# Optimization experiments

Measured on AMD Instinct MI355X. Metric: run time of the kernel, lower is better.

## Reference

```python
import jax, jax.numpy as jnp
import numpy as np

N, F, H, K, E = 10000, 128, 128, 500, 320000
EPS = 1e-15


def setup_inputs() -> dict:
    key = jax.random.key(0)
    ks = jax.random.split(key, 16)
    def lin(k, fi, fo):
        return jax.random.normal(k, (fi, fo), jnp.float32) / np.sqrt(fi).astype(np.float32)
    inp = {
        'nodes': jax.random.normal(ks[0], (N, F), jnp.float32),
        'edges': jax.random.randint(ks[1], (2, E), 0, N, jnp.int32),
        'batch': jnp.zeros((N,), jnp.int32),
        'W1': lin(ks[2], F, H), 'b1': jnp.zeros((H,), jnp.float32),
        'W2': lin(ks[3], H, H), 'b2': jnp.zeros((H,), jnp.float32),
        'pool_W': lin(ks[4], H, K), 'pool_b': jnp.zeros((K,), jnp.float32),
        'W3': lin(ks[5], H, H), 'b3': jnp.zeros((H,), jnp.float32),
        'W4': lin(ks[6], H, H), 'b4': jnp.zeros((H,), jnp.float32),
        'W5': lin(ks[7], H, F), 'b5': jnp.zeros((F,), jnp.float32),
    }
    return inp


def reference(nodes, edges, batch, W1, b1, W2, b2, pool_W, pool_b, W3, b3, W4, b4, W5, b5):
    n = nodes.shape[0]
    row, col = edges[0], edges[1]
    # GCN normalization with self-loops (computed once, shared by all convs)
    loop = jnp.arange(n, dtype=row.dtype)
    row_sl = jnp.concatenate([row, loop])
    col_sl = jnp.concatenate([col, loop])
    deg = jax.ops.segment_sum(jnp.ones_like(col_sl, dtype=nodes.dtype), col_sl, num_segments=n)
    dinv = jnp.where(deg > 0, 1.0 / jnp.sqrt(deg), 0.0)
    norm = dinv[row_sl] * dinv[col_sl]  # [E+N]

    def gcn(x, W, b):
        h = x @ W
        msg = h[row_sl] * norm[:, None]
        return jax.ops.segment_sum(msg, col_sl, num_segments=n) + b

    x = jnp.tanh(gcn(nodes, W1, b1))
    x = jnp.tanh(gcn(x, W2, b2))

    # dense batch (single graph) + dense adjacency [1, N, N]
    adj = jnp.zeros((n, n), x.dtype).at[row, col].add(1.0)[None]
    xd = x[None]                                   # [1, N, H]
    s_logits = xd @ pool_W + pool_b                # [1, N, K]

    # ---- dense_mincut_pool ----
    s = jax.nn.softmax(s_logits, axis=-1)
    k = s.shape[-1]
    out = jnp.einsum('bnk,bnh->bkh', s, xd)        # s^T x, [1, K, H]
    a_s = adj @ s                                  # [1, N, K]
    out_adj = jnp.swapaxes(s, 1, 2) @ a_s          # s^T A s, [1, K, K]
    mincut_num = jnp.trace(out_adj, axis1=1, axis2=2)
    d_flat = adj.sum(-1)                           # [1, N]
    # trace(s^T D s) = sum_n d_n * sum_k s_nk^2
    mincut_den = jnp.einsum('bn,bnk,bnk->b', d_flat, s, s) + EPS
    mincut_loss = jnp.mean(-(mincut_num / mincut_den))
    ss = jnp.swapaxes(s, 1, 2) @ s                 # [1, K, K]
    ss_norm = jnp.linalg.norm(ss, axis=(-1, -2), keepdims=True)
    i_s_normed = jnp.eye(k, dtype=ss.dtype) / jnp.sqrt(jnp.asarray(k, ss.dtype))
    ortho_loss = jnp.mean(jnp.linalg.norm(ss / (ss_norm + EPS) - i_s_normed, axis=(-1, -2)))
    # zero diagonal, then symmetric degree normalization
    out_adj = out_adj * (1.0 - jnp.eye(k, dtype=out_adj.dtype))
    d = jnp.sqrt(out_adj.sum(-1))[:, None] + EPS   # [1, 1, K]
    out_adj = out_adj / d / jnp.swapaxes(d, 1, 2)
    # ---- end pool ----

    s2 = jax.nn.softmax(s_logits, axis=-1)
    x_out = (s2 @ out)[0]                          # [N, H]
    adj_out = s2 @ (out_adj @ jnp.swapaxes(s2, 1, 2))  # [1, N, N]

    # recon_adj = False -> reuse original edge_index
    x = jnp.tanh(gcn(x_out, W3, b3))
    x = jnp.tanh(gcn(x, W4, b4))
    x = gcn(x, W5, b5)
    return x, adj_out, mincut_loss, ortho_loss
```

## Files before the change

kernel.cpp:

```cpp
#include <hip/hip_runtime.h>
#include <hip/hip_bf16.h>
#include <math.h>

#define EPSF 1e-15f

typedef __attribute__((ext_vector_type(8))) short bf16x8;
typedef __attribute__((ext_vector_type(4))) float f32x4;

__device__ __forceinline__ void gload_lds16(const void* g, void* l){
  __builtin_amdgcn_global_load_lds(
    (const __attribute__((address_space(1))) unsigned int*)(g),
    (__attribute__((address_space(3))) unsigned int*)(l), 16, 0, 0);
}


__global__ void k_count_deg(const int* __restrict__ edges, int E, int* indeg, int* outdeg){
  int e = blockIdx.x*blockDim.x + threadIdx.x;
  if (e >= E) return;
  int r = edges[e], c = edges[E+e];
  atomicAdd(&outdeg[r], 1);
  atomicAdd(&indeg[c], 1);
}

__global__ void k_dinv(const int* __restrict__ indeg, float* __restrict__ dinv, int N){
  int i = blockIdx.x*blockDim.x + threadIdx.x;
  if (i >= N) return;
  dinv[i] = rsqrtf((float)(indeg[i] + 1));
}

__global__ void k_scan_block(const int* __restrict__ cnt, int* __restrict__ rowptr, int n){
  __shared__ int csum[257];
  const int T = 256;
  int chunk = (n + T - 1)/T;
  int t = threadIdx.x;
  int beg = t*chunk, end = min(n, beg + chunk);
  int s = 0;
  for (int i = beg; i < end; ++i) s += cnt[i];
  csum[t+1] = s;
  if (t == 0) csum[0] = 0;
  __syncthreads();
  if (t == 0){ for (int i = 1; i <= T; ++i) csum[i] += csum[i-1]; }
  __syncthreads();
  int acc = csum[t];
  for (int i = beg; i < end; ++i){ rowptr[i] = acc; acc += cnt[i]; }
  if (t == T-1) rowptr[n] = csum[T];
}

__global__ void k_fill_csr(const int* __restrict__ edges, int E, int* cur_in, int* cur_out,
                           int* __restrict__ src, int* __restrict__ dst){
  int e = blockIdx.x*blockDim.x + threadIdx.x;
  if (e >= E) return;
  int r = edges[e], c = edges[E+e];
  int p = atomicAdd(&cur_in[c], 1);  src[p] = r;
  int q = atomicAdd(&cur_out[r], 1); dst[q] = c;
}

__global__ __launch_bounds__(128)
void k_gcn_agg_b(const __hip_bfloat16* __restrict__ hb, const float* __restrict__ dinv,
                 const int* __restrict__ rowptr, const int* __restrict__ src,
                 const float* __restrict__ bias, float* __restrict__ outf,
                 __hip_bfloat16* __restrict__ outb, int Hd, int do_tanh){
  int c = blockIdx.x;
  int t = threadIdx.x;
  float dc = dinv[c];
  float sum = __bfloat162float(hb[(size_t)c*Hd + t]) * dc;
  int e0 = rowptr[c], e1 = rowptr[c+1];
  for (int e = e0; e < e1; ++e){
    int sidx = src[e];
    sum += __bfloat162float(hb[(size_t)sidx*Hd + t]) * dinv[sidx];
  }
  float v = sum * dc + bias[t];
  if (do_tanh) v = tanhf(v);
  if (outf) outf[(size_t)c*Hd + t] = v;
  if (outb) outb[(size_t)c*Hd + t] = __float2bfloat16(v);
}

__global__ __launch_bounds__(256)
void k_as_agg_b2(const __hip_bfloat16* __restrict__ sb, const int* __restrict__ rowptr,
                 const int* __restrict__ dst, float* __restrict__ a_s, int K2, int KP2){
  int n = blockIdx.x;
  int e0 = rowptr[n], e1 = rowptr[n+1];
  const unsigned* sb32 = (const unsigned*)sb;
  for (int k = threadIdx.x; k < K2; k += blockDim.x){
    float a0 = 0.f, a1 = 0.f;
    for (int e = e0; e < e1; ++e){
      unsigned v = sb32[(size_t)dst[e]*KP2 + k];
      a0 += __uint_as_float(v << 16);
      a1 += __uint_as_float(v & 0xFFFF0000u);
    }
    float2* o = (float2*)(a_s + (size_t)n*(K2*2));
    o[k] = make_float2(a0, a1);
  }
}

__global__ void k_pack_bf16pad(const float* __restrict__ x, __hip_bfloat16* __restrict__ y,
                               int rows, int K, int KP){
  long long n = (long long)rows*KP;
  for (long long i = (long long)blockIdx.x*blockDim.x + threadIdx.x; i < n;
       i += (long long)gridDim.x*blockDim.x){
    int row = (int)(i / KP), col = (int)(i - (long long)row*KP);
    y[i] = (col < K) ? __float2bfloat16(x[(size_t)row*K + col]) : __float2bfloat16(0.f);
  }
}

__global__ __launch_bounds__(256)
void k_transpose_f2b(const float* __restrict__ X, __hip_bfloat16* __restrict__ XT,
                     int R, int C, int Cp, int Np){
  __shared__ float t[32][33];
  int jb = blockIdx.x*32;
  int ib = blockIdx.y*32;
  int tx = threadIdx.x & 31, ty = threadIdx.x >> 5;
  #pragma unroll
  for (int k = 0; k < 4; ++k){
    int i = ib + ty + k*8, j = jb + tx;
    t[ty + k*8][tx] = (i < R && j < C) ? X[(size_t)i*C + j] : 0.f;
  }
  __syncthreads();
  #pragma unroll
  for (int k = 0; k < 4; ++k){
    int jr = jb + ty + k*8, ic = ib + tx;
    if (jr < Cp && ic < Np)
      XT[(size_t)jr*Np + ic] = __float2bfloat16(t[tx][ty + k*8]);
  }
}

#define MT 128
#define NT 128
#define KT 32
__global__ __launch_bounds__(256)
void k_gemm_abt_mfma(const short* __restrict__ A, const short* __restrict__ B,
                     const float* __restrict__ bias,
                     float* __restrict__ Cf, __hip_bfloat16* __restrict__ Cb,
                     int M, int Nd, int KP, int ldcb, int swz){
  __shared__ __align__(16) short Asl[128*32];
  __shared__ __align__(16) short Bsl[128*32];
  int bx = blockIdx.x, by = blockIdx.y;
  if (swz){
    int gx = gridDim.x;
    int nwg = gx * gridDim.y;
    int bid = by*gx + bx;
    int q = nwg >> 3, r = nwg & 7;
    int xcd = bid & 7, o = bid >> 3;
    int nb = (xcd < r ? xcd*(q+1) : r*(q+1) + (xcd - r)*q) + o;
    bx = nb % gx; by = nb / gx;
  }
  int tid = threadIdx.x;
  int lane = tid & 63, wave = tid >> 6;
  int wr = wave >> 1, wc = wave & 1;
  int l15 = lane & 15, l4 = lane >> 4;
  int tM = by * MT, tN = bx * NT;

  f32x4 acc[4][4];
  #pragma unroll
  for (int i = 0; i < 4; ++i)
    #pragma unroll
    for (int j = 0; j < 4; ++j) acc[i][j] = (f32x4){0.f,0.f,0.f,0.f};

  const short* gA0 = A + (size_t)(tM + (tid>>2))*KP + (tid&3)*8;
  const short* gA1 = A + (size_t)(tM + 64 + (tid>>2))*KP + (tid&3)*8;
  const short* gB0 = B + (size_t)(tN + (tid>>2))*KP + (tid&3)*8;
  const short* gB1 = B + (size_t)(tN + 64 + (tid>>2))*KP + (tid&3)*8;
  short* lA0 = Asl + wave*512;
  short* lA1 = Asl + 2048 + wave*512;
  short* lB0 = Bsl + wave*512;
  short* lB1 = Bsl + 2048 + wave*512;

  for (int k0 = 0; k0 < KP; k0 += KT){
    __syncthreads();
    gload_lds16(gA0 + k0, lA0);
    gload_lds16(gA1 + k0, lA1);
    gload_lds16(gB0 + k0, lB0);
    gload_lds16(gB1 + k0, lB1);
    __syncthreads();

    bf16x8 af[4], bfr[4];
    #pragma unroll
    for (int mi = 0; mi < 4; ++mi)
      af[mi] = *(const bf16x8*)(Asl + (wr*64 + mi*16 + l15)*32 + l4*8);
    #pragma unroll
    for (int nj = 0; nj < 4; ++nj)
      bfr[nj] = *(const bf16x8*)(Bsl + (wc*64 + nj*16 + l15)*32 + l4*8);
    #pragma unroll
    for (int mi = 0; mi < 4; ++mi)
      #pragma unroll
      for (int nj = 0; nj < 4; ++nj)
        acc[mi][nj] = __builtin_amdgcn_mfma_f32_16x16x32_bf16(af[mi], bfr[nj], acc[mi][nj], 0, 0, 0);
  }

  #pragma unroll
  for (int mi = 0; mi < 4; ++mi){
    #pragma unroll
    for (int r = 0; r < 4; ++r){
      int gr = tM + wr*64 + mi*16 + l4*4 + r;
      if (gr >= M) continue;
      #pragma unroll
      for (int nj = 0; nj < 4; ++nj){
        int gc = tN + wc*64 + nj*16 + l15;
        if (gc >= Nd) continue;
        float v = acc[mi][nj][r];
        if (bias) v += bias[gc];
        if (Cf) Cf[(size_t)gr*Nd + gc] = v;
        else    Cb[(size_t)gr*ldcb + gc] = __float2bfloat16(v);
      }
    }
  }
}

__global__ __launch_bounds__(256)
void k_gemm_abt_mfma_sk(const short* __restrict__ A, const short* __restrict__ B,
                        float* __restrict__ C, int M, int Nd, int ldC,
                        int KL, int kChunk){
  __shared__ __align__(16) short Asl[128*32];
  __shared__ __align__(16) short Bsl[128*32];
  int tid = threadIdx.x;
  int lane = tid & 63, wave = tid >> 6;
  int wr = wave >> 1, wc = wave & 1;
  int l15 = lane & 15, l4 = lane >> 4;
  int tM = blockIdx.y * MT, tN = blockIdx.x * NT;
  int kBeg = blockIdx.z * kChunk;
  int kEnd = min(KL, kBeg + kChunk);

  f32x4 acc[4][4];
  #pragma unroll
  for (int i = 0; i < 4; ++i)
    #pragma unroll
    for (int j = 0; j < 4; ++j) acc[i][j] = (f32x4){0.f,0.f,0.f,0.f};

  const short* gA0 = A + (size_t)(tM + (tid>>2))*KL + (tid&3)*8;
  const short* gA1 = A + (size_t)(tM + 64 + (tid>>2))*KL + (tid&3)*8;
  const short* gB0 = B + (size_t)(tN + (tid>>2))*KL + (tid&3)*8;
  const short* gB1 = B + (size_t)(tN + 64 + (tid>>2))*KL + (tid&3)*8;
  short* lA0 = Asl + wave*512;
  short* lA1 = Asl + 2048 + wave*512;
  short* lB0 = Bsl + wave*512;
  short* lB1 = Bsl + 2048 + wave*512;

  for (int k0 = kBeg; k0 < kEnd; k0 += KT){
    __syncthreads();
    gload_lds16(gA0 + k0, lA0);
    gload_lds16(gA1 + k0, lA1);
    gload_lds16(gB0 + k0, lB0);
    gload_lds16(gB1 + k0, lB1);
    __syncthreads();

    bf16x8 af[4], bfr[4];
    #pragma unroll
    for (int mi = 0; mi < 4; ++mi)
      af[mi] = *(const bf16x8*)(Asl + (wr*64 + mi*16 + l15)*32 + l4*8);
    #pragma unroll
    for (int nj = 0; nj < 4; ++nj)
      bfr[nj] = *(const bf16x8*)(Bsl + (wc*64 + nj*16 + l15)*32 + l4*8);
    #pragma unroll
    for (int mi = 0; mi < 4; ++mi)
      #pragma unroll
      for (int nj = 0; nj < 4; ++nj)
        acc[mi][nj] = __builtin_amdgcn_mfma_f32_16x16x32_bf16(af[mi], bfr[nj], acc[mi][nj], 0, 0, 0);
  }

  #pragma unroll
  for (int mi = 0; mi < 4; ++mi){
    #pragma unroll
    for (int r = 0; r < 4; ++r){
      int gr = tM + wr*64 + mi*16 + l4*4 + r;
      if (gr >= M) continue;
      #pragma unroll
      for (int nj = 0; nj < 4; ++nj){
        int gc = tN + wc*64 + nj*16 + l15;
        if (gc >= Nd) continue;
        atomicAdd(&C[(size_t)gr*ldC + gc], acc[mi][nj][r]);
      }
    }
  }
}


__global__ __launch_bounds__(256)
void k_softmax(float* __restrict__ s, __hip_bfloat16* __restrict__ sb,
               const int* __restrict__ outdeg,
               float* __restrict__ scalars, int N, int K, int KP){
  int wid = threadIdx.x >> 6, lane = threadIdx.x & 63;
  int row = blockIdx.x*4 + wid;
  if (row >= N) return;
  float* sr = s + (size_t)row*K;
  __hip_bfloat16* sbr = sb + (size_t)row*KP;
  float v[8];
  float m = -INFINITY;
  #pragma unroll
  for (int i = 0; i < 8; ++i){
    int k = lane + i*64;
    v[i] = (k < K) ? sr[k] : -INFINITY;
    m = fmaxf(m, v[i]);
  }
  for (int off = 32; off; off >>= 1) m = fmaxf(m, __shfl_xor(m, off));
  float sum = 0.f;
  #pragma unroll
  for (int i = 0; i < 8; ++i){
    int k = lane + i*64;
    if (k < K){ v[i] = expf(v[i] - m); sum += v[i]; } else v[i] = 0.f;
  }
  for (int off = 32; off; off >>= 1) sum += __shfl_xor(sum, off);
  float inv = 1.f / sum;
  float ssq = 0.f;
  #pragma unroll
  for (int i = 0; i < 8; ++i){
    int k = lane + i*64;
    if (k < K){
      float p = v[i]*inv;
      sr[k] = p;
      sbr[k] = __float2bfloat16(p);
      ssq += p*p;
    }
  }
  for (int off = 32; off; off >>= 1) ssq += __shfl_xor(ssq, off);
  if (lane == 0) atomicAdd(&scalars[1], (float)outdeg[row] * ssq);
}

__global__ void k_trace(const float* __restrict__ P, float* __restrict__ scalars, int K){
  float t = 0.f;
  for (int i = threadIdx.x; i < K; i += blockDim.x) t += P[(size_t)i*K + i];
  for (int off = 32; off; off >>= 1) t += __shfl_xor(t, off);
  __shared__ float wsum[4];
  int lane = threadIdx.x & 63, wid = threadIdx.x >> 6;
  if (lane == 0) wsum[wid] = t;
  __syncthreads();
  if (threadIdx.x == 0) scalars[0] = wsum[0]+wsum[1]+wsum[2]+wsum[3];
}

__global__ void k_reduce_sq(const float* __restrict__ x, int n, float* __restrict__ out){
  float a = 0.f;
  for (int i = blockIdx.x*blockDim.x + threadIdx.x; i < n; i += gridDim.x*blockDim.x){
    float v = x[i]; a += v*v;
  }
  for (int off = 32; off; off >>= 1) a += __shfl_xor(a, off);
  if ((threadIdx.x & 63) == 0) atomicAdd(out, a);
}

__global__ void k_ortho(const float* __restrict__ ss, const float* __restrict__ scalars,
                        int K, float* __restrict__ out){
  float inv = 1.f / (sqrtf(scalars[2]) + EPSF);
  float isk = rsqrtf((float)K);
  float a = 0.f;
  int n = K*K;
  for (int idx = blockIdx.x*blockDim.x + threadIdx.x; idx < n; idx += gridDim.x*blockDim.x){
    int i = idx / K, j = idx - i*K;
    float v = ss[idx]*inv - ((i == j) ? isk : 0.f);
    a += v*v;
  }
  for (int off = 32; off; off >>= 1) a += __shfl_xor(a, off);
  if ((threadIdx.x & 63) == 0) atomicAdd(out, a);
}

__global__ __launch_bounds__(256)
void k_rowsum_d(const float* __restrict__ P, float* __restrict__ dvec, int K){
  int wid = threadIdx.x >> 6, lane = threadIdx.x & 63;
  int row = blockIdx.x*4 + wid;
  if (row >= K) return;
  const float* pr = P + (size_t)row*K;
  float rs = 0.f;
  for (int j = lane; j < K; j += 64) if (j != row) rs += pr[j];
  for (int off = 32; off; off >>= 1) rs += __shfl_xor(rs, off);
  if (lane == 0) dvec[row] = sqrtf(rs) + EPSF;
}

__global__ void k_norm_adj(float* __restrict__ P, const float* __restrict__ dvec, int K){
  int idx = blockIdx.x*blockDim.x + threadIdx.x;
  if (idx >= K*K) return;
  int i = idx / K, j = idx - i*K;
  float v = P[idx];
  P[idx] = (i == j) ? 0.f : v / (dvec[i]*dvec[j]);
}

__global__ void k_finalize(const float* __restrict__ scalars, float* __restrict__ out2){
  if (threadIdx.x == 0){
    out2[0] = -(scalars[0] / (scalars[1] + EPSF));
    out2[1] = sqrtf(scalars[3]);
  }
}


extern "C" void kernel_launch(void* const* d_in, const int* in_sizes, int n_in,
                              void* d_out, int out_size, void* d_ws, size_t ws_size,
                              hipStream_t stream) {
  const float* nodes = (const float*)d_in[0];
  const int*   edges = (const int*)d_in[1];
  const float* W1 = (const float*)d_in[3];  const float* b1 = (const float*)d_in[4];
  const float* W2 = (const float*)d_in[5];  const float* b2 = (const float*)d_in[6];
  const float* pW = (const float*)d_in[7];  const float* pB = (const float*)d_in[8];
  const float* W3 = (const float*)d_in[9];  const float* b3 = (const float*)d_in[10];
  const float* W4 = (const float*)d_in[11]; const float* b4 = (const float*)d_in[12];
  const float* W5 = (const float*)d_in[13]; const float* b5 = (const float*)d_in[14];

  const int H = 128, F = 128, N = 10000, E = 320000, K = 500;
  const int KP = 512;
  const int NP = 10016;
  const int MP = 79*128;
  (void)n_in; (void)out_size; (void)in_sizes;

  float* out_x   = (float*)d_out;
  float* out_adj = out_x + (size_t)N*F;
  float* out_ls  = out_adj + (size_t)N*N;

  char* ws = (char*)d_ws;
  size_t off = 0;
  auto alloc = [&](size_t bytes) -> void* {
    off = (off + 255) & ~(size_t)255;
    void* p = ws + off;
    off += bytes;
    return p;
  };
  int*   deg2       = (int*)alloc((size_t)2*N*4);
  int*   indeg      = deg2;
  int*   outdeg     = deg2 + N;
  float* zf         = (float*)alloc(((size_t)K*H + 2*(size_t)K*K + 64)*4);
  float* out_pool   = zf;
  float* P          = zf + (size_t)K*H;
  float* ssm        = P + (size_t)K*K;
  float* scalars    = ssm + (size_t)K*K;
  __hip_bfloat16* sub = (__hip_bfloat16*)alloc((size_t)2*MP*KP*2);
  __hip_bfloat16* s_b = sub;
  __hip_bfloat16* u_b = sub + (size_t)MP*KP;
  int*   rowptr_in  = (int*)alloc((size_t)(N+1)*4);
  int*   rowptr_out = (int*)alloc((size_t)(N+1)*4);
  int*   cur_in     = (int*)alloc((size_t)N*4);
  int*   cur_out    = (int*)alloc((size_t)N*4);
  int*   csr_src    = (int*)alloc((size_t)E*4);
  int*   csr_dst    = (int*)alloc((size_t)E*4);
  float* dinv       = (float*)alloc((size_t)N*4);
  __hip_bfloat16* h_b  = (__hip_bfloat16*)alloc((size_t)N*H*2);
  __hip_bfloat16* nodes_b = (__hip_bfloat16*)alloc((size_t)MP*H*2);
  __hip_bfloat16* xa_b = (__hip_bfloat16*)alloc((size_t)MP*H*2);
  __hip_bfloat16* xb_b = (__hip_bfloat16*)alloc((size_t)MP*H*2);
  float* xb         = (float*)alloc((size_t)N*H*4);
  float* s          = (float*)alloc((size_t)N*K*4);
  float* a_s        = (float*)alloc((size_t)N*K*4);
  float* dvec       = (float*)alloc((size_t)K*4);
  __hip_bfloat16* Pt_b = (__hip_bfloat16*)alloc((size_t)KP*KP*2);
  __hip_bfloat16* st_b = (__hip_bfloat16*)alloc((size_t)KP*NP*2);
  __hip_bfloat16* a_st = (__hip_bfloat16*)alloc((size_t)KP*NP*2);
  __hip_bfloat16* xbt  = (__hip_bfloat16*)alloc((size_t)H*NP*2);
  __hip_bfloat16* opT  = (__hip_bfloat16*)alloc((size_t)H*KP*2);
  __hip_bfloat16* W1t  = (__hip_bfloat16*)alloc((size_t)H*F*2);
  __hip_bfloat16* W2t  = (__hip_bfloat16*)alloc((size_t)H*H*2);
  __hip_bfloat16* W3t  = (__hip_bfloat16*)alloc((size_t)H*H*2);
  __hip_bfloat16* W4t  = (__hip_bfloat16*)alloc((size_t)H*H*2);
  __hip_bfloat16* W5t  = (__hip_bfloat16*)alloc((size_t)F*H*2);
  __hip_bfloat16* pWt  = (__hip_bfloat16*)alloc((size_t)KP*H*2);
  (void)ws_size;

  hipMemsetAsync(deg2, 0, (size_t)2*N*4, stream);
  hipMemsetAsync(zf,   0, ((size_t)K*H + 2*(size_t)K*K + 64)*4, stream);
  hipMemsetAsync(sub,  0, (size_t)2*MP*KP*2, stream);

  int eb = (E + 255)/256;
  k_count_deg<<<eb, 256, 0, stream>>>(edges, E, indeg, outdeg);
  k_dinv<<<(N+255)/256, 256, 0, stream>>>(indeg, dinv, N);
  k_scan_block<<<1, 256, 0, stream>>>(indeg,  rowptr_in,  N);
  k_scan_block<<<1, 256, 0, stream>>>(outdeg, rowptr_out, N);
  hipMemcpyAsync(cur_in,  rowptr_in,  (size_t)N*4, hipMemcpyDeviceToDevice, stream);
  hipMemcpyAsync(cur_out, rowptr_out, (size_t)N*4, hipMemcpyDeviceToDevice, stream);
  k_fill_csr<<<eb, 256, 0, stream>>>(edges, E, cur_in, cur_out, csr_src, csr_dst);

  { dim3 g(4, 4);  k_transpose_f2b<<<g, 256, 0, stream>>>(W1, W1t, F, H, H, F); }
  { dim3 g(4, 4);  k_transpose_f2b<<<g, 256, 0, stream>>>(W2, W2t, H, H, H, H); }
  { dim3 g(4, 4);  k_transpose_f2b<<<g, 256, 0, stream>>>(W3, W3t, H, H, H, H); }
  { dim3 g(4, 4);  k_transpose_f2b<<<g, 256, 0, stream>>>(W4, W4t, H, H, H, H); }
  { dim3 g(4, 4);  k_transpose_f2b<<<g, 256, 0, stream>>>(W5, W5t, H, F, F, H); }
  { dim3 g(16, 4); k_transpose_f2b<<<g, 256, 0, stream>>>(pW, pWt, H, K, KP, H); }
  k_pack_bf16pad<<<1024, 256, 0, stream>>>(nodes, nodes_b, N, F, F);

  auto mfma = [&](const __hip_bfloat16* A, const __hip_bfloat16* B, const float* bias,
                  float* Cf, __hip_bfloat16* Cb, int M, int Nd, int Kp, int ldcb, int swz){
    dim3 g((Nd + NT - 1)/NT, (M + MT - 1)/MT);
    k_gemm_abt_mfma<<<g, 256, 0, stream>>>((const short*)A, (const short*)B, bias,
                                           Cf, Cb, M, Nd, Kp, ldcb, swz);
  };

  mfma(nodes_b, W1t, nullptr, nullptr, h_b, N, H, F, H, 0);
  k_gcn_agg_b<<<N, H, 0, stream>>>(h_b, dinv, rowptr_in, csr_src, b1, nullptr, xa_b, H, 1);
  mfma(xa_b, W2t, nullptr, nullptr, h_b, N, H, H, H, 0);
  k_gcn_agg_b<<<N, H, 0, stream>>>(h_b, dinv, rowptr_in, csr_src, b2, xb, xb_b, H, 1);

  mfma(xb_b, pWt, pB, s, nullptr, N, K, H, 0, 0);
  k_softmax<<<(N+3)/4, 256, 0, stream>>>(s, s_b, outdeg, scalars, N, K, KP);
  { dim3 g(KP/32, NP/32); k_transpose_f2b<<<g, 256, 0, stream>>>(s,   st_b, N, K, KP, NP); }
  k_as_agg_b2<<<N, 256, 0, stream>>>(s_b, rowptr_out, csr_dst, a_s, K/2, KP/2);
  { dim3 g(KP/32, NP/32); k_transpose_f2b<<<g, 256, 0, stream>>>(a_s, a_st, N, K, KP, NP); }
  { dim3 g(H/32,  NP/32); k_transpose_f2b<<<g, 256, 0, stream>>>(xb,  xbt,  N, H, H,  NP); }

  const int kChunk = 1280;
  { dim3 g(1, 4, 8); k_gemm_abt_mfma_sk<<<g, 256, 0, stream>>>((const short*)st_b, (const short*)xbt,
                                                               out_pool, K, H, H, NP, kChunk); }
  { dim3 g(4, 4, 8); k_gemm_abt_mfma_sk<<<g, 256, 0, stream>>>((const short*)st_b, (const short*)a_st,
                                                               P, K, K, K, NP, kChunk); }
  { dim3 g(4, 4, 8); k_gemm_abt_mfma_sk<<<g, 256, 0, stream>>>((const short*)st_b, (const short*)st_b,
                                                               ssm, K, K, K, NP, kChunk); }
  k_trace<<<1, 256, 0, stream>>>(P, scalars, K);
  k_reduce_sq<<<256, 256, 0, stream>>>(ssm, K*K, &scalars[2]);
  k_ortho<<<256, 256, 0, stream>>>(ssm, scalars, K, &scalars[3]);
  k_rowsum_d<<<(K+3)/4, 256, 0, stream>>>(P, dvec, K);
  k_norm_adj<<<(K*K+255)/256, 256, 0, stream>>>(P, dvec, K);
  k_finalize<<<1, 64, 0, stream>>>(scalars, out_ls);

  { dim3 g(KP/32, KP/32); k_transpose_f2b<<<g, 256, 0, stream>>>(P, Pt_b, K, K, KP, KP); }
  mfma(s_b, Pt_b, nullptr, nullptr, u_b, N, K, KP, KP, 0);
  mfma(u_b, s_b, nullptr, out_adj, nullptr, N, N, KP, 0, 1);
  { dim3 g(H/32, KP/32); k_transpose_f2b<<<g, 256, 0, stream>>>(out_pool, opT, K, H, H, KP); }
  mfma(s_b, opT, nullptr, nullptr, xa_b, N, H, KP, H, 0);

  mfma(xa_b, W3t, nullptr, nullptr, h_b, N, H, H, H, 0);
  k_gcn_agg_b<<<N, H, 0, stream>>>(h_b, dinv, rowptr_in, csr_src, b3, nullptr, xb_b, H, 1);
  mfma(xb_b, W4t, nullptr, nullptr, h_b, N, H, H, H, 0);
  k_gcn_agg_b<<<N, H, 0, stream>>>(h_b, dinv, rowptr_in, csr_src, b4, nullptr, xa_b, H, 1);
  mfma(xa_b, W5t, nullptr, nullptr, h_b, N, F, H, F, 0);
  k_gcn_agg_b<<<N, F, 0, stream>>>(h_b, dinv, rowptr_in, csr_src, b5, out_x, nullptr, F, 0);
}
```

Baseline: 1.021 ms.

## Batch small kernels and fuse pooling split-K GEMMs to cut launch overhead

Merges many small launches. The dinv computation and cursor copies are folded into the scan kernel. The six weight transposes become one batched launch, and two of the N-sized transposes become another. The three split-K pooling GEMMs run as a single grid, and the trace, reduce, ortho and adjacency-normalisation kernels are combined into two stats kernels. The GCN aggregation loop is also unrolled by two with dual accumulators to expose more memory parallelism. The goal is fewer launches and host API calls. The cost is branchy dispatch and some idle blocks in the batched grids.

```diff
diff --git a/kernel.cpp b/kernel.cpp
--- a/kernel.cpp
+++ b/kernel.cpp
@@ -22,13 +22,8 @@
   atomicAdd(&indeg[c], 1);
 }
 
-__global__ void k_dinv(const int* __restrict__ indeg, float* __restrict__ dinv, int N){
-  int i = blockIdx.x*blockDim.x + threadIdx.x;
-  if (i >= N) return;
-  dinv[i] = rsqrtf((float)(indeg[i] + 1));
-}
-
-__global__ void k_scan_block(const int* __restrict__ cnt, int* __restrict__ rowptr, int n){
+__global__ void k_scan_fused(const int* __restrict__ cnt, int* __restrict__ rowptr,
+                             int* __restrict__ cur, float* __restrict__ dinvOut, int n){
   __shared__ int csum[257];
   const int T = 256;
   int chunk = (n + T - 1)/T;
@@ -42,7 +37,12 @@
   if (t == 0){ for (int i = 1; i <= T; ++i) csum[i] += csum[i-1]; }
   __syncthreads();
   int acc = csum[t];
-  for (int i = beg; i < end; ++i){ rowptr[i] = acc; acc += cnt[i]; }
+  for (int i = beg; i < end; ++i){
+    rowptr[i] = acc;
+    cur[i] = acc;
+    if (dinvOut) dinvOut[i] = rsqrtf((float)(cnt[i] + 1));
+    acc += cnt[i];
+  }
   if (t == T-1) rowptr[n] = csum[T];
 }
 
@@ -64,11 +64,19 @@
   int t = threadIdx.x;
   float dc = dinv[c];
   float sum = __bfloat162float(hb[(size_t)c*Hd + t]) * dc;
+  float sum2 = 0.f;
   int e0 = rowptr[c], e1 = rowptr[c+1];
-  for (int e = e0; e < e1; ++e){
-    int sidx = src[e];
-    sum += __bfloat162float(hb[(size_t)sidx*Hd + t]) * dinv[sidx];
-  }
+  int e = e0;
+  for (; e + 1 < e1; e += 2){
+    int sa = src[e], sb2 = src[e+1];
+    sum  += __bfloat162float(hb[(size_t)sa*Hd  + t]) * dinv[sa];
+    sum2 += __bfloat162float(hb[(size_t)sb2*Hd + t]) * dinv[sb2];
+  }
+  if (e < e1){
+    int sa = src[e];
+    sum += __bfloat162float(hb[(size_t)sa*Hd + t]) * dinv[sa];
+  }
+  sum += sum2;
   float v = sum * dc + bias[t];
   if (do_tanh) v = tanhf(v);
   if (outf) outf[(size_t)c*Hd + t] = v;
@@ -103,12 +111,12 @@
   }
 }
 
-__global__ __launch_bounds__(256)
-void k_transpose_f2b(const float* __restrict__ X, __hip_bfloat16* __restrict__ XT,
-                     int R, int C, int Cp, int Np){
+__device__ __forceinline__ void transpose_tile(const float* X, __hip_bfloat16* XT,
+                                               int R, int C, int Cp, int Np,
+                                               int bx, int by){
   __shared__ float t[32][33];
-  int jb = blockIdx.x*32;
-  int ib = blockIdx.y*32;
+  int jb = bx*32;
+  int ib = by*32;
   int tx = threadIdx.x & 31, ty = threadIdx.x >> 5;
   #pragma unroll
   for (int k = 0; k < 4; ++k){
@@ -122,6 +130,38 @@
     if (jr < Cp && ic < Np)
       XT[(size_t)jr*Np + ic] = __float2bfloat16(t[tx][ty + k*8]);
   }
+}
+
+__global__ __launch_bounds__(256)
+void k_transpose_f2b(const float* __restrict__ X, __hip_bfloat16* __restrict__ XT,
+                     int R, int C, int Cp, int Np){
+  transpose_tile(X, XT, R, C, Cp, Np, blockIdx.x, blockIdx.y);
+}
+
+struct TPar { const float* src; __hip_bfloat16* dst; int R, C, Cp, Np; };
+
+__global__ __launch_bounds__(256)
+void k_transpose_batch6(TPar p0, TPar p1, TPar p2, TPar p3, TPar p4, TPar p5){
+  TPar p;
+  switch (blockIdx.z){
+    case 0: p = p0; break;
+    case 1: p = p1; break;
+    case 2: p = p2; break;
+    case 3: p = p3; break;
+    case 4: p = p4; break;
+    default: p = p5; break;
+  }
+  if ((int)blockIdx.x >= (p.Cp + 31)/32 || (int)blockIdx.y >= (p.Np + 31)/32) return;
+  transpose_tile(p.src, p.dst, p.R, p.C, p.Cp, p.Np, blockIdx.x, blockIdx.y);
+}
+
+__global__ __launch_bounds__(256)
+void k_transpose_batch2(const float* __restrict__ X0, __hip_bfloat16* __restrict__ T0,
+                        const float* __restrict__ X1, __hip_bfloat16* __restrict__ T1,
+                        int R, int C, int Cp, int Np){
+  const float* X = blockIdx.z ? X1 : X0;
+  __hip_bfloat16* XT = blockIdx.z ? T1 : T0;
+  transpose_tile(X, XT, R, C, Cp, Np, blockIdx.x, blockIdx.y);
 }
 
 #define MT 128
@@ -207,17 +247,24 @@
 }
 
 __global__ __launch_bounds__(256)
-void k_gemm_abt_mfma_sk(const short* __restrict__ A, const short* __restrict__ B,
-                        float* __restrict__ C, int M, int Nd, int ldC,
-                        int KL, int kChunk){
+void k_pool_sk(const short* __restrict__ st, const short* __restrict__ xbt,
+               const short* __restrict__ a_st,
+               float* __restrict__ out_pool, float* __restrict__ P, float* __restrict__ ssm,
+               int K, int Hd, int KL, int kChunk){
   __shared__ __align__(16) short Asl[128*32];
   __shared__ __align__(16) short Bsl[128*32];
+  int sel = blockIdx.z >> 3;
+  int chunk = blockIdx.z & 7;
+  const short* B = (sel == 0) ? xbt : (sel == 1) ? a_st : st;
+  float* C = (sel == 0) ? out_pool : (sel == 1) ? P : ssm;
+  int Nd = (sel == 0) ? Hd : K;
+  if ((int)blockIdx.x * NT >= ((sel == 0) ? Hd : 512)) return;
   int tid = threadIdx.x;
   int lane = tid & 63, wave = tid >> 6;
   int wr = wave >> 1, wc = wave & 1;
   int l15 = lane & 15, l4 = lane >> 4;
   int tM = blockIdx.y * MT, tN = blockIdx.x * NT;
-  int kBeg = blockIdx.z * kChunk;
+  int kBeg = chunk * kChunk;
   int kEnd = min(KL, kBeg + kChunk);
 
   f32x4 acc[4][4];
@@ -226,8 +273,8 @@
     #pragma unroll
     for (int j = 0; j < 4; ++j) acc[i][j] = (f32x4){0.f,0.f,0.f,0.f};
 
-  const short* gA0 = A + (size_t)(tM + (tid>>2))*KL + (tid&3)*8;
-  const short* gA1 = A + (size_t)(tM + 64 + (tid>>2))*KL + (tid&3)*8;
+  const short* gA0 = st + (size_t)(tM + (tid>>2))*KL + (tid&3)*8;
+  const short* gA1 = st + (size_t)(tM + 64 + (tid>>2))*KL + (tid&3)*8;
   const short* gB0 = B + (size_t)(tN + (tid>>2))*KL + (tid&3)*8;
   const short* gB1 = B + (size_t)(tN + 64 + (tid>>2))*KL + (tid&3)*8;
   short* lA0 = Asl + wave*512;
@@ -262,12 +309,12 @@
     #pragma unroll
     for (int r = 0; r < 4; ++r){
       int gr = tM + wr*64 + mi*16 + l4*4 + r;
-      if (gr >= M) continue;
+      if (gr >= K) continue;
       #pragma unroll
       for (int nj = 0; nj < 4; ++nj){
         int gc = tN + wc*64 + nj*16 + l15;
         if (gc >= Nd) continue;
-        atomicAdd(&C[(size_t)gr*ldC + gc], acc[mi][nj][r]);
+        atomicAdd(&C[(size_t)gr*Nd + gc], acc[mi][nj][r]);
       }
     }
   }
@@ -315,39 +362,23 @@
   if (lane == 0) atomicAdd(&scalars[1], (float)outdeg[row] * ssq);
 }
 
-__global__ void k_trace(const float* __restrict__ P, float* __restrict__ scalars, int K){
-  float t = 0.f;
-  for (int i = threadIdx.x; i < K; i += blockDim.x) t += P[(size_t)i*K + i];
-  for (int off = 32; off; off >>= 1) t += __shfl_xor(t, off);
-  __shared__ float wsum[4];
-  int lane = threadIdx.x & 63, wid = threadIdx.x >> 6;
-  if (lane == 0) wsum[wid] = t;
-  __syncthreads();
-  if (threadIdx.x == 0) scalars[0] = wsum[0]+wsum[1]+wsum[2]+wsum[3];
-}
-
-__global__ void k_reduce_sq(const float* __restrict__ x, int n, float* __restrict__ out){
-  float a = 0.f;
-  for (int i = blockIdx.x*blockDim.x + threadIdx.x; i < n; i += gridDim.x*blockDim.x){
-    float v = x[i]; a += v*v;
-  }
-  for (int off = 32; off; off >>= 1) a += __shfl_xor(a, off);
-  if ((threadIdx.x & 63) == 0) atomicAdd(out, a);
-}
-
-__global__ void k_ortho(const float* __restrict__ ss, const float* __restrict__ scalars,
-                        int K, float* __restrict__ out){
-  float inv = 1.f / (sqrtf(scalars[2]) + EPSF);
-  float isk = rsqrtf((float)K);
-  float a = 0.f;
+__global__ void k_stats1(const float* __restrict__ P, const float* __restrict__ ssm,
+                         float* __restrict__ scalars, int K){
+  float tr = 0.f, sq = 0.f;
   int n = K*K;
   for (int idx = blockIdx.x*blockDim.x + threadIdx.x; idx < n; idx += gridDim.x*blockDim.x){
+    float v = ssm[idx]; sq += v*v;
     int i = idx / K, j = idx - i*K;
-    float v = ss[idx]*inv - ((i == j) ? isk : 0.f);
-    a += v*v;
-  }
-  for (int off = 32; off; off >>= 1) a += __shfl_xor(a, off);
-  if ((threadIdx.x & 63) == 0) atomicAdd(out, a);
+    if (i == j) tr += P[idx];
+  }
+  for (int off = 32; off; off >>= 1){
+    tr += __shfl_xor(tr, off);
+    sq += __shfl_xor(sq, off);
+  }
+  if ((threadIdx.x & 63) == 0){
+    if (tr != 0.f) atomicAdd(&scalars[0], tr);
+    atomicAdd(&scalars[2], sq);
+  }
 }
 
 __global__ __launch_bounds__(256)
@@ -362,12 +393,22 @@
   if (lane == 0) dvec[row] = sqrtf(rs) + EPSF;
 }
 
-__global__ void k_norm_adj(float* __restrict__ P, const float* __restrict__ dvec, int K){
-  int idx = blockIdx.x*blockDim.x + threadIdx.x;
-  if (idx >= K*K) return;
-  int i = idx / K, j = idx - i*K;
-  float v = P[idx];
-  P[idx] = (i == j) ? 0.f : v / (dvec[i]*dvec[j]);
+__global__ void k_stats2(float* __restrict__ P, const float* __restrict__ ssm,
+                         const float* __restrict__ dvec,
+                         const float* __restrict__ scalars, float* __restrict__ out3, int K){
+  float inv = 1.f / (sqrtf(scalars[2]) + EPSF);
+  float isk = rsqrtf((float)K);
+  float a = 0.f;
+  int n = K*K;
+  for (int idx = blockIdx.x*blockDim.x + threadIdx.x; idx < n; idx += gridDim.x*blockDim.x){
+    int i = idx / K, j = idx - i*K;
+    float v = ssm[idx]*inv - ((i == j) ? isk : 0.f);
+    a += v*v;
+    float pv = P[idx];
+    P[idx] = (i == j) ? 0.f : pv / (dvec[i]*dvec[j]);
+  }
+  for (int off = 32; off; off >>= 1) a += __shfl_xor(a, off);
+  if ((threadIdx.x & 63) == 0) atomicAdd(out3, a);
 }
 
 __global__ void k_finalize(const float* __restrict__ scalars, float* __restrict__ out2){
@@ -453,19 +494,20 @@
 
   int eb = (E + 255)/256;
   k_count_deg<<<eb, 256, 0, stream>>>(edges, E, indeg, outdeg);
-  k_dinv<<<(N+255)/256, 256, 0, stream>>>(indeg, dinv, N);
-  k_scan_block<<<1, 256, 0, stream>>>(indeg,  rowptr_in,  N);
-  k_scan_block<<<1, 256, 0, stream>>>(outdeg, rowptr_out, N);
-  hipMemcpyAsync(cur_in,  rowptr_in,  (size_t)N*4, hipMemcpyDeviceToDevice, stream);
-  hipMemcpyAsync(cur_out, rowptr_out, (size_t)N*4, hipMemcpyDeviceToDevice, stream);
+  k_scan_fused<<<1, 256, 0, stream>>>(indeg,  rowptr_in,  cur_in,  dinv,    N);
+  k_scan_fused<<<1, 256, 0, stream>>>(outdeg, rowptr_out, cur_out, nullptr, N);
   k_fill_csr<<<eb, 256, 0, stream>>>(edges, E, cur_in, cur_out, csr_src, csr_dst);
 
-  { dim3 g(4, 4);  k_transpose_f2b<<<g, 256, 0, stream>>>(W1, W1t, F, H, H, F); }
-  { dim3 g(4, 4);  k_transpose_f2b<<<g, 256, 0, stream>>>(W2, W2t, H, H, H, H); }
-  { dim3 g(4, 4);  k_transpose_f2b<<<g, 256, 0, stream>>>(W3, W3t, H, H, H, H); }
-  { dim3 g(4, 4);  k_transpose_f2b<<<g, 256, 0, stream>>>(W4, W4t, H, H, H, H); }
-  { dim3 g(4, 4);  k_transpose_f2b<<<g, 256, 0, stream>>>(W5, W5t, H, F, F, H); }
-  { dim3 g(16, 4); k_transpose_f2b<<<g, 256, 0, stream>>>(pW, pWt, H, K, KP, H); }
+  {
+    TPar p0 = { W1, W1t, F, H, H, F };
+    TPar p1 = { W2, W2t, H, H, H, H };
+    TPar p2 = { W3, W3t, H, H, H, H };
+    TPar p3 = { W4, W4t, H, H, H, H };
+    TPar p4 = { W5, W5t, H, F, F, H };
+    TPar p5 = { pW, pWt, H, K, KP, H };
+    dim3 g(16, 4, 6);
+    k_transpose_batch6<<<g, 256, 0, stream>>>(p0, p1, p2, p3, p4, p5);
+  }
   k_pack_bf16pad<<<1024, 256, 0, stream>>>(nodes, nodes_b, N, F, F);
 
   auto mfma = [&](const __hip_bfloat16* A, const __hip_bfloat16* B, const float* bias,
@@ -482,23 +524,17 @@
 
   mfma(xb_b, pWt, pB, s, nullptr, N, K, H, 0, 0);
   k_softmax<<<(N+3)/4, 256, 0, stream>>>(s, s_b, outdeg, scalars, N, K, KP);
-  { dim3 g(KP/32, NP/32); k_transpose_f2b<<<g, 256, 0, stream>>>(s,   st_b, N, K, KP, NP); }
   k_as_agg_b2<<<N, 256, 0, stream>>>(s_b, rowptr_out, csr_dst, a_s, K/2, KP/2);
-  { dim3 g(KP/32, NP/32); k_transpose_f2b<<<g, 256, 0, stream>>>(a_s, a_st, N, K, KP, NP); }
-  { dim3 g(H/32,  NP/32); k_transpose_f2b<<<g, 256, 0, stream>>>(xb,  xbt,  N, H, H,  NP); }
+  { dim3 g(KP/32, NP/32, 2); k_transpose_batch2<<<g, 256, 0, stream>>>(s, st_b, a_s, a_st, N, K, KP, NP); }
+  { dim3 g(H/32, NP/32); k_transpose_f2b<<<g, 256, 0, stream>>>(xb, xbt, N, H, H, NP); }
 
   const int kChunk = 1280;
-  { dim3 g(1, 4, 8); k_gemm_abt_mfma_sk<<<g, 256, 0, stream>>>((const short*)st_b, (const short*)xbt,
-                                                               out_pool, K, H, H, NP, kChunk); }
-  { dim3 g(4, 4, 8); k_gemm_abt_mfma_sk<<<g, 256, 0, stream>>>((const short*)st_b, (const short*)a_st,
-                                                               P, K, K, K, NP, kChunk); }
-  { dim3 g(4, 4, 8); k_gemm_abt_mfma_sk<<<g, 256, 0, stream>>>((const short*)st_b, (const short*)st_b,
-                                                               ssm, K, K, K, NP, kChunk); }
-  k_trace<<<1, 256, 0, stream>>>(P, scalars, K);
-  k_reduce_sq<<<256, 256, 0, stream>>>(ssm, K*K, &scalars[2]);
-  k_ortho<<<256, 256, 0, stream>>>(ssm, scalars, K, &scalars[3]);
+  { dim3 g(4, 4, 24); k_pool_sk<<<g, 256, 0, stream>>>((const short*)st_b, (const short*)xbt,
+                                                       (const short*)a_st,
+                                                       out_pool, P, ssm, K, H, NP, kChunk); }
+  k_stats1<<<128, 256, 0, stream>>>(P, ssm, scalars, K);
   k_rowsum_d<<<(K+3)/4, 256, 0, stream>>>(P, dvec, K);
-  k_norm_adj<<<(K*K+255)/256, 256, 0, stream>>>(P, dvec, K);
+  k_stats2<<<128, 256, 0, stream>>>(P, ssm, dvec, scalars, &scalars[3], K);
   k_finalize<<<1, 64, 0, stream>>>(scalars, out_ls);
 
   { dim3 g(KP/32, KP/32); k_transpose_f2b<<<g, 256, 0, stream>>>(P, Pt_b, K, K, KP, KP); }
```

Measured after the change: 900.3 us. 1.13x faster.
